# Kernel tuning notes

Hardware: AMD Instinct MI355X
Metric: run time of the kernel (lower is better)

The kernel has to match this reference:

```python
import jax, jax.numpy as jnp
import numpy as np

B, T, H, N_CLASSES = 2048, 128, 64, 32
N_STEPS = 10  # euler micro-steps over t in [0,1], step_size=0.1


def setup_inputs() -> dict:
    key = jax.random.key(0)
    ks = jax.random.split(key, 16)
    s = lambda fan_in: 1.0 / np.sqrt(fan_in)
    inp = {
        "times": jax.random.uniform(ks[0], (B, T), jnp.float32),
        "marks": jax.random.randint(ks[1], (B, T, 1), 0, N_CLASSES),
        "mask": jnp.ones((B, T), jnp.float32),
        # Diffeq.net: MLP(H+1 -> H -> H -> H), Tanh activations, Tanh final
        "W0": jax.random.uniform(ks[2], (H, H + 1), jnp.float32, -s(H + 1), s(H + 1)),
        "b0": jax.random.uniform(ks[3], (H,), jnp.float32, -s(H + 1), s(H + 1)),
        "W1": jax.random.uniform(ks[4], (H, H), jnp.float32, -s(H), s(H)),
        "b1": jax.random.uniform(ks[5], (H,), jnp.float32, -s(H), s(H)),
        "W2": jax.random.uniform(ks[6], (H, H), jnp.float32, -s(H), s(H)),
        "b2": jax.random.uniform(ks[7], (H,), jnp.float32, -s(H), s(H)),
        # Diffeq.intensity: Linear(H -> 1) + Softplus
        "Wi": jax.random.uniform(ks[8], (1, H), jnp.float32, -s(H), s(H)),
        "bi": jax.random.uniform(ks[9], (1,), jnp.float32, -s(H), s(H)) + 0.5,
        # Embedding(n_classes, H)
        "emb": jax.random.normal(ks[10], (N_CLASSES, H), jnp.float32),
        # LSTMCell(1+H, H)
        "W_ih": jax.random.uniform(ks[11], (4 * H, 1 + H), jnp.float32, -s(H), s(H)),
        "W_hh": jax.random.uniform(ks[12], (4 * H, H), jnp.float32, -s(H), s(H)),
        "b_ih": jax.random.uniform(ks[13], (4 * H,), jnp.float32, -s(H), s(H)),
        "b_hh": jax.random.uniform(ks[14], (4 * H,), jnp.float32, -s(H), s(H)),
    }
    return inp


def reference(times, marks, mask, W0, b0, W1, b1, W2, b2, Wi, bi, emb,
              W_ih, W_hh, b_ih, b_hh):
    dt = jnp.float32(1.0 / N_STEPS)

    def mlp(x):  # Diffeq.net
        x = jnp.tanh(x @ W0.T + b0)
        x = jnp.tanh(x @ W1.T + b1)
        return jnp.tanh(x @ W2.T + b2)

    def intensity(h):  # Diffeq.intensity (Softplus head) -> (B,1)
        return jax.nn.softplus(h @ Wi.T + bi)

    # faithful to original: marks[:, 1] is used at every timestep
    m1 = emb[marks[:, 1, 0]]  # (B,H)

    def step(carry, t_col):
        h, c = carry                       # (B,H), (B,H)
        t = t_col[:, None]                 # (B,1) -- diff (event time)
        # fixed-step euler solve of the Diffeq over s in [0,1]
        def euler(state, s):
            hh, integ = state
            s_t = (s * dt) * t             # (B,1) integration time scaled
            d_h = mlp(jnp.concatenate([s_t, hh], -1)) * t
            d_i = intensity(hh) * t
            return (hh + dt * d_h, integ + dt * d_i), None
        (h_ode, integ), _ = jax.lax.scan(
            euler, (h, jnp.zeros_like(t)),
            jnp.arange(N_STEPS, dtype=times.dtype))
        inten = intensity(h_ode)           # (B,1)
        # LSTMCell update with input [t, mark_embedding]
        x_in = jnp.concatenate([t, m1], -1)           # (B,1+H)
        gates = x_in @ W_ih.T + b_ih + h_ode @ W_hh.T + b_hh
        i_g, f_g, g_g, o_g = jnp.split(gates, 4, -1)
        c_new = jax.nn.sigmoid(f_g) * c + jax.nn.sigmoid(i_g) * jnp.tanh(g_g)
        h_new = jax.nn.sigmoid(o_g) * jnp.tanh(c_new)
        nll = (-jnp.log(inten) + integ)[:, 0]          # (B,)
        return (h_new, c_new), (h_ode, nll)

    h0 = jnp.zeros((times.shape[0], emb.shape[1]), times.dtype)
    _, (hidden, nll) = jax.lax.scan(step, (h0, h0), times.T)
    hidden = jnp.transpose(hidden, (1, 0, 2))   # (B,T,H)
    nll = nll.T                                  # (B,T)
    loss = (nll * mask).sum() / mask.sum()
    return loss, hidden
```

## Files before the change

### kernel.cpp

```cpp
#include <hip/hip_runtime.h>


#define T_LEN 128

typedef float  f32x4  __attribute__((ext_vector_type(4)));
typedef __bf16 bf16x8 __attribute__((ext_vector_type(8)));
typedef __bf16 bf16x2 __attribute__((ext_vector_type(2)));

#define MFMA16(a, b, c) __builtin_amdgcn_mfma_f32_16x16x32_bf16((a), (b), (c), 0, 0, 0)

__device__ __forceinline__ float rcp_f(float x) { return __builtin_amdgcn_rcpf(x); }
__device__ __forceinline__ float exp2_f(float x) { return __builtin_amdgcn_exp2f(x); }
__device__ __forceinline__ float log2_f(float x) { return __builtin_amdgcn_logf(x); }

constexpr float kL2E = 1.44269504088896340736f;
constexpr float kLN2 = 0.69314718055994530942f;

__device__ __forceinline__ float tanh_fast(float x) {
  float e = exp2_f(x * (2.0f * kL2E));
  return 1.0f - 2.0f * rcp_f(e + 1.0f);
}
__device__ __forceinline__ float sigm_fast(float x) {
  return rcp_f(1.0f + exp2_f(-kL2E * x));
}
__device__ __forceinline__ float softplus_fast(float x) {
  float neg = log2_f(1.0f + exp2_f(-kL2E * fabsf(x))) * kLN2;
  return fmaxf(x, 0.0f) + neg;
}
__device__ __forceinline__ unsigned packbf(float a, float b) {
  bf16x2 v; v[0] = (__bf16)a; v[1] = (__bf16)b;
  return __builtin_bit_cast(unsigned, v);
}

__launch_bounds__(256)
__global__ void jumpode_main(
    const float* __restrict__ times, const int* __restrict__ marks,
    const float* __restrict__ maskp, const float* __restrict__ W0,
    const float* __restrict__ b0,    const float* __restrict__ W1,
    const float* __restrict__ b1,    const float* __restrict__ W2,
    const float* __restrict__ b2,    const float* __restrict__ Wi,
    const float* __restrict__ bi,    const float* __restrict__ emb,
    const float* __restrict__ W_ih,  const float* __restrict__ W_hh,
    const float* __restrict__ b_ih,  const float* __restrict__ b_hh,
    float* __restrict__ out, float* __restrict__ ws)
{
  __shared__ __align__(16) unsigned whh_l[256 * 32];
  __shared__ __align__(16) float    gm1_l[8 * 256];
  __shared__ __align__(16) unsigned xbuf[2][16 * 32];
  __shared__ __align__(16) float    pint[16 * 4];
  __shared__ __align__(16) float    b0_l[64], b1_l[64], b2_l[64];
  __shared__ __align__(16) float    w0c0_l[64];
  __shared__ __align__(16) float    wihc0_l[256];
  __shared__ __align__(16) float    emb16[8][64];

  const int tid = threadIdx.x;
  const int wv  = tid >> 6;
  const int l   = tid & 63;
  const int b   = l & 15;
  const int q   = l >> 4;
  const int bm  = b & 7;
  const int row = blockIdx.x * 8 + bm;
  const int xsw = b & 7;

  if (tid < 64) {
    b0_l[tid] = b0[tid]; b1_l[tid] = b1[tid]; b2_l[tid] = b2[tid];
    w0c0_l[tid] = W0[tid * 65];
  }
  wihc0_l[tid] = W_ih[tid * 65];
  for (int idx = tid; idx < 512; idx += 256) {
    int rr = idx >> 6, cc = idx & 63;
    int mk = marks[(blockIdx.x * 8 + rr) * T_LEN + 1];
    emb16[rr][cc] = emb[mk * 64 + cc];
  }
  #pragma unroll 4
  for (int i = 0; i < 32; ++i) {
    int idx = i * 256 + tid;
    int rw = idx >> 5, c2 = idx & 31;
    unsigned pw = packbf(W_hh[rw * 64 + 2 * c2], W_hh[rw * 64 + 2 * c2 + 1]);
    int gr = c2 >> 2;
    whh_l[rw * 32 + ((gr ^ (rw & 7)) << 2) + (c2 & 3)] = pw;
  }
  __syncthreads();

  {
    int g = tid;
    float acc[8];
    #pragma unroll
    for (int bb = 0; bb < 8; ++bb) acc[bb] = 0.0f;
    const float* wr = &W_ih[g * 65 + 1];
    for (int k = 0; k < 64; ++k) {
      float w = wr[k];
      #pragma unroll
      for (int bb = 0; bb < 8; ++bb) acc[bb] += w * emb16[bb][k];
    }
    float bias = b_ih[g] + b_hh[g];
    int gg = g >> 2;
    #pragma unroll
    for (int bb = 0; bb < 8; ++bb)
      gm1_l[bb * 256 + ((gg ^ bb) << 2) + (g & 3)] = acc[bb] + bias;
  }

  bf16x8 w0f[2], w1f[2], w2f[2];
  {
    const int fm = 16 * wv + b;
    #pragma unroll
    for (int kt = 0; kt < 2; ++kt) {
      const float* r0 = &W0[fm * 65 + 1 + kt * 32 + q * 8];
      const float* r1 = &W1[fm * 64 +     kt * 32 + q * 8];
      const float* r2 = &W2[fm * 64 +     kt * 32 + q * 8];
      bf16x8 a, bb, c;
      #pragma unroll
      for (int e = 0; e < 8; ++e) {
        a[e] = (__bf16)r0[e]; bb[e] = (__bf16)r1[e]; c[e] = (__bf16)r2[e];
      }
      w0f[kt] = a; w1f[kt] = bb; w2f[kt] = c;
    }
  }
  f32x4 wiv;
  #pragma unroll
  for (int r = 0; r < 4; ++r) wiv[r] = Wi[16 * wv + 4 * q + r];
  const float bi_s = bi[0];
  const f32x4 b0v = *(const f32x4*)&b0_l[16 * wv + 4 * q];
  const f32x4 b1v = *(const f32x4*)&b1_l[16 * wv + 4 * q];
  const f32x4 b2v = *(const f32x4*)&b2_l[16 * wv + 4 * q];
  const f32x4 c0v = *(const f32x4*)&w0c0_l[16 * wv + 4 * q];
  __syncthreads();

  auto write_x = [&](unsigned* buf, const f32x4 v) {
    int gr = (2 * wv + (q >> 1)) ^ xsw;
    int wb = b * 32 + (gr << 2) + ((q & 1) << 1);
    buf[wb]     = packbf(v[0], v[1]);
    buf[wb + 1] = packbf(v[2], v[3]);
  };
  auto read_bfrag = [&](const unsigned* buf, int kt) -> bf16x8 {
    int gr = (kt * 4 + q) ^ xsw;
    return *(const bf16x8*)((const char*)buf + b * 128 + gr * 16);
  };
  auto whh_frag = [&](int R, int kt) -> bf16x8 {
    int rw = R * 16 + b;
    int gr = (kt * 4 + q) ^ xsw;
    return *(const bf16x8*)((const char*)whh_l + rw * 128 + gr * 16);
  };
  auto ld_gm1 = [&](int R) -> f32x4 {
    int gr = (R * 4 + q) ^ xsw;
    return *(const f32x4*)((const char*)gm1_l + bm * 1024 + gr * 16);
  };
  auto isect_partial = [&](const f32x4 v) {
    float part = wiv[0] * v[0] + wiv[1] * v[1] + wiv[2] * v[2] + wiv[3] * v[3];
    part += __shfl_xor(part, 16);
    part += __shfl_xor(part, 32);
    if (l < 16) pint[b * 4 + wv] = part;
  };

  f32x4 hst = (f32x4){0.f, 0.f, 0.f, 0.f};
  f32x4 cst = (f32x4){0.f, 0.f, 0.f, 0.f};
  float nll_acc = 0.f, m_acc = 0.f;
  const float sel0 = (q == 0 && b < 8) ? 1.0f : 0.0f;
  int xp = 0;

  #pragma unroll 1
  for (int step = 0; step < T_LEN; ++step) {
    const float tb  = times[row * T_LEN + step];
    const float dtt = 0.1f * tb;
    f32x4 hh = hst;
    float integ = 0.f;

    #pragma unroll 1
    for (int s = 0; s < 10; ++s) {
      isect_partial(hh);
      write_x(xbuf[xp], hh);
      __syncthreads();
      bf16x8 Bf0 = read_bfrag(xbuf[xp], 0), Bf1 = read_bfrag(xbuf[xp], 1);
      xp ^= 1;
      if (wv == 0) {
        f32x4 p = *(const f32x4*)&pint[b * 4];
        integ += dtt * softplus_fast(p[0] + p[1] + p[2] + p[3] + bi_s);
      }
      const float st = (float)s * dtt;

      f32x4 acc = (f32x4){0.f, 0.f, 0.f, 0.f};
      acc = MFMA16(w0f[0], Bf0, acc);
      acc = MFMA16(w0f[1], Bf1, acc);
      f32x4 y;
      #pragma unroll
      for (int r = 0; r < 4; ++r) y[r] = tanh_fast(acc[r] + b0v[r] + c0v[r] * st);
      write_x(xbuf[xp], y);
      __syncthreads();
      Bf0 = read_bfrag(xbuf[xp], 0); Bf1 = read_bfrag(xbuf[xp], 1);
      xp ^= 1;

      acc = (f32x4){0.f, 0.f, 0.f, 0.f};
      acc = MFMA16(w1f[0], Bf0, acc);
      acc = MFMA16(w1f[1], Bf1, acc);
      #pragma unroll
      for (int r = 0; r < 4; ++r) y[r] = tanh_fast(acc[r] + b1v[r]);
      write_x(xbuf[xp], y);
      __syncthreads();
      Bf0 = read_bfrag(xbuf[xp], 0); Bf1 = read_bfrag(xbuf[xp], 1);
      xp ^= 1;

      acc = (f32x4){0.f, 0.f, 0.f, 0.f};
      acc = MFMA16(w2f[0], Bf0, acc);
      acc = MFMA16(w2f[1], Bf1, acc);
      #pragma unroll
      for (int r = 0; r < 4; ++r) hh[r] += dtt * tanh_fast(acc[r] + b2v[r]);
    }

    isect_partial(hh);
    write_x(xbuf[xp], hh);
    if (b < 8) {
      size_t obase = 1 + (((size_t)row) * T_LEN + step) * 64 + 16 * wv + 4 * q;
      out[obase + 0] = hh[0]; out[obase + 1] = hh[1];
      out[obase + 2] = hh[2]; out[obase + 3] = hh[3];
    }
    __syncthreads();
    bf16x8 Bf0 = read_bfrag(xbuf[xp], 0), Bf1 = read_bfrag(xbuf[xp], 1);
    xp ^= 1;

    float nll = 0.f;
    if (wv == 0) {
      f32x4 p = *(const f32x4*)&pint[b * 4];
      float inten = softplus_fast(p[0] + p[1] + p[2] + p[3] + bi_s);
      nll = -(log2_f(inten) * kLN2) + integ;
    }

    f32x4 ga[4];
    #pragma unroll
    for (int g = 0; g < 4; ++g) {
      const int Rb = 4 * g + wv;
      f32x4 a = (f32x4){0.f, 0.f, 0.f, 0.f};
      a = MFMA16(whh_frag(Rb, 0), Bf0, a);
      a = MFMA16(whh_frag(Rb, 1), Bf1, a);
      f32x4 gm = ld_gm1(Rb);
      f32x4 wc = *(const f32x4*)&wihc0_l[Rb * 16 + q * 4];
      #pragma unroll
      for (int r = 0; r < 4; ++r) ga[g][r] = a[r] + gm[r] + wc[r] * tb;
    }
    #pragma unroll
    for (int r = 0; r < 4; ++r) {
      float ig = sigm_fast(ga[0][r]), fg = sigm_fast(ga[1][r]);
      float gg = tanh_fast(ga[2][r]), og = sigm_fast(ga[3][r]);
      float cn = fg * cst[r] + ig * gg;
      cst[r] = cn;
      hst[r] = og * tanh_fast(cn);
    }

    if (wv == 0) {
      float mval = maskp[row * T_LEN + step];
      nll_acc += sel0 * mval * nll;
      m_acc   += sel0 * mval;
    }
  }

  if (wv == 0) {
    #pragma unroll
    for (int off = 1; off < 64; off <<= 1) {
      nll_acc += __shfl_xor(nll_acc, off);
      m_acc   += __shfl_xor(m_acc, off);
    }
    if (tid == 0) {
      atomicAdd(&ws[0], nll_acc);
      atomicAdd(&ws[1], m_acc);
    }
  }
}

__global__ void jumpode_fin(const float* __restrict__ ws, float* __restrict__ out) {
  if (threadIdx.x == 0 && blockIdx.x == 0) out[0] = ws[0] / ws[1];
}

extern "C" void kernel_launch(void* const* d_in, const int* in_sizes, int n_in,
                              void* d_out, int out_size, void* d_ws, size_t ws_size,
                              hipStream_t stream) {
  (void)in_sizes; (void)n_in; (void)out_size; (void)ws_size;
  const float* times = (const float*)d_in[0];
  const int*   marks = (const int*)  d_in[1];
  const float* maskp = (const float*)d_in[2];
  const float* W0    = (const float*)d_in[3];
  const float* b0    = (const float*)d_in[4];
  const float* W1    = (const float*)d_in[5];
  const float* b1    = (const float*)d_in[6];
  const float* W2    = (const float*)d_in[7];
  const float* b2    = (const float*)d_in[8];
  const float* Wi    = (const float*)d_in[9];
  const float* bi    = (const float*)d_in[10];
  const float* emb   = (const float*)d_in[11];
  const float* W_ih  = (const float*)d_in[12];
  const float* W_hh  = (const float*)d_in[13];
  const float* b_ih  = (const float*)d_in[14];
  const float* b_hh  = (const float*)d_in[15];
  float* out = (float*)d_out;
  float* ws  = (float*)d_ws;

  (void)hipMemsetAsync(d_ws, 0, 2 * sizeof(float), stream);
  jumpode_main<<<dim3(256), dim3(256), 0, stream>>>(
      times, marks, maskp, W0, b0, W1, b1, W2, b2, Wi, bi, emb,
      W_ih, W_hh, b_ih, b_hh, out, ws);
  jumpode_fin<<<dim3(1), dim3(64), 0, stream>>>(ws, out);
}
```

Baseline: 1.006 ms.

## Halve batch rows per block to 4, double grid, fold biases into MFMA accumulators

Each block now handles 4 batch rows instead of 8, and the grid doubles to 512 blocks so more CUs take part in the serial recurrence. The 16-wide MFMA N dimension is now only a quarter used, but per-block latency is unchanged while the parallel spread over the 256 CUs doubles. Bias and time terms are preloaded into the MFMA accumulator input, which removes per-element adds after the matrix ops. The cost is that each block repeats its weight staging into LDS and registers, and less of each MFMA does useful work.

```diff
diff --git a/kernel.cpp b/kernel.cpp
--- a/kernel.cpp
+++ b/kernel.cpp
@@ -45,21 +45,21 @@
     float* __restrict__ out, float* __restrict__ ws)
 {
   __shared__ __align__(16) unsigned whh_l[256 * 32];
-  __shared__ __align__(16) float    gm1_l[8 * 256];
+  __shared__ __align__(16) float    gm1_l[4 * 256];
   __shared__ __align__(16) unsigned xbuf[2][16 * 32];
   __shared__ __align__(16) float    pint[16 * 4];
   __shared__ __align__(16) float    b0_l[64], b1_l[64], b2_l[64];
   __shared__ __align__(16) float    w0c0_l[64];
   __shared__ __align__(16) float    wihc0_l[256];
-  __shared__ __align__(16) float    emb16[8][64];
+  __shared__ __align__(16) float    emb16[4][64];
 
   const int tid = threadIdx.x;
   const int wv  = tid >> 6;
   const int l   = tid & 63;
   const int b   = l & 15;
   const int q   = l >> 4;
-  const int bm  = b & 7;
-  const int row = blockIdx.x * 8 + bm;
+  const int bm  = b & 3;
+  const int row = blockIdx.x * 4 + bm;
   const int xsw = b & 7;
 
   if (tid < 64) {
@@ -67,9 +67,9 @@
     w0c0_l[tid] = W0[tid * 65];
   }
   wihc0_l[tid] = W_ih[tid * 65];
-  for (int idx = tid; idx < 512; idx += 256) {
-    int rr = idx >> 6, cc = idx & 63;
-    int mk = marks[(blockIdx.x * 8 + rr) * T_LEN + 1];
+  if (tid < 256) {
+    int rr = tid >> 6, cc = tid & 63;
+    int mk = marks[(blockIdx.x * 4 + rr) * T_LEN + 1];
     emb16[rr][cc] = emb[mk * 64 + cc];
   }
   #pragma unroll 4
@@ -84,19 +84,19 @@
 
   {
     int g = tid;
-    float acc[8];
-    #pragma unroll
-    for (int bb = 0; bb < 8; ++bb) acc[bb] = 0.0f;
+    float acc[4];
+    #pragma unroll
+    for (int bb = 0; bb < 4; ++bb) acc[bb] = 0.0f;
     const float* wr = &W_ih[g * 65 + 1];
     for (int k = 0; k < 64; ++k) {
       float w = wr[k];
       #pragma unroll
-      for (int bb = 0; bb < 8; ++bb) acc[bb] += w * emb16[bb][k];
+      for (int bb = 0; bb < 4; ++bb) acc[bb] += w * emb16[bb][k];
     }
     float bias = b_ih[g] + b_hh[g];
     int gg = g >> 2;
     #pragma unroll
-    for (int bb = 0; bb < 8; ++bb)
+    for (int bb = 0; bb < 4; ++bb)
       gm1_l[bb * 256 + ((gg ^ bb) << 2) + (g & 3)] = acc[bb] + bias;
   }
 
@@ -142,7 +142,7 @@
     return *(const bf16x8*)((const char*)whh_l + rw * 128 + gr * 16);
   };
   auto ld_gm1 = [&](int R) -> f32x4 {
-    int gr = (R * 4 + q) ^ xsw;
+    int gr = (R * 4 + q) ^ bm;
     return *(const f32x4*)((const char*)gm1_l + bm * 1024 + gr * 16);
   };
   auto isect_partial = [&](const f32x4 v) {
@@ -155,7 +155,7 @@
   f32x4 hst = (f32x4){0.f, 0.f, 0.f, 0.f};
   f32x4 cst = (f32x4){0.f, 0.f, 0.f, 0.f};
   float nll_acc = 0.f, m_acc = 0.f;
-  const float sel0 = (q == 0 && b < 8) ? 1.0f : 0.0f;
+  const float sel0 = (q == 0 && b < 4) ? 1.0f : 0.0f;
   int xp = 0;
 
   #pragma unroll 1
@@ -178,37 +178,37 @@
       }
       const float st = (float)s * dtt;
 
-      f32x4 acc = (f32x4){0.f, 0.f, 0.f, 0.f};
-      acc = MFMA16(w0f[0], Bf0, acc);
+      f32x4 cin;
+      #pragma unroll
+      for (int r = 0; r < 4; ++r) cin[r] = b0v[r] + c0v[r] * st;
+      f32x4 acc = MFMA16(w0f[0], Bf0, cin);
       acc = MFMA16(w0f[1], Bf1, acc);
       f32x4 y;
       #pragma unroll
-      for (int r = 0; r < 4; ++r) y[r] = tanh_fast(acc[r] + b0v[r] + c0v[r] * st);
+      for (int r = 0; r < 4; ++r) y[r] = tanh_fast(acc[r]);
       write_x(xbuf[xp], y);
       __syncthreads();
       Bf0 = read_bfrag(xbuf[xp], 0); Bf1 = read_bfrag(xbuf[xp], 1);
       xp ^= 1;
 
-      acc = (f32x4){0.f, 0.f, 0.f, 0.f};
-      acc = MFMA16(w1f[0], Bf0, acc);
+      acc = MFMA16(w1f[0], Bf0, b1v);
       acc = MFMA16(w1f[1], Bf1, acc);
       #pragma unroll
-      for (int r = 0; r < 4; ++r) y[r] = tanh_fast(acc[r] + b1v[r]);
+      for (int r = 0; r < 4; ++r) y[r] = tanh_fast(acc[r]);
       write_x(xbuf[xp], y);
       __syncthreads();
       Bf0 = read_bfrag(xbuf[xp], 0); Bf1 = read_bfrag(xbuf[xp], 1);
       xp ^= 1;
 
-      acc = (f32x4){0.f, 0.f, 0.f, 0.f};
-      acc = MFMA16(w2f[0], Bf0, acc);
+      acc = MFMA16(w2f[0], Bf0, b2v);
       acc = MFMA16(w2f[1], Bf1, acc);
       #pragma unroll
-      for (int r = 0; r < 4; ++r) hh[r] += dtt * tanh_fast(acc[r] + b2v[r]);
+      for (int r = 0; r < 4; ++r) hh[r] += dtt * tanh_fast(acc[r]);
     }
 
     isect_partial(hh);
     write_x(xbuf[xp], hh);
-    if (b < 8) {
+    if (b < 4) {
       size_t obase = 1 + (((size_t)row) * T_LEN + step) * 64 + 16 * wv + 4 * q;
       out[obase + 0] = hh[0]; out[obase + 1] = hh[1];
       out[obase + 2] = hh[2]; out[obase + 3] = hh[3];
@@ -228,13 +228,13 @@
     #pragma unroll
     for (int g = 0; g < 4; ++g) {
       const int Rb = 4 * g + wv;
-      f32x4 a = (f32x4){0.f, 0.f, 0.f, 0.f};
-      a = MFMA16(whh_frag(Rb, 0), Bf0, a);
-      a = MFMA16(whh_frag(Rb, 1), Bf1, a);
       f32x4 gm = ld_gm1(Rb);
       f32x4 wc = *(const f32x4*)&wihc0_l[Rb * 16 + q * 4];
-      #pragma unroll
-      for (int r = 0; r < 4; ++r) ga[g][r] = a[r] + gm[r] + wc[r] * tb;
+      f32x4 cin;
+      #pragma unroll
+      for (int r = 0; r < 4; ++r) cin[r] = gm[r] + wc[r] * tb;
+      f32x4 a = MFMA16(whh_frag(Rb, 0), Bf0, cin);
+      ga[g] = MFMA16(whh_frag(Rb, 1), Bf1, a);
     }
     #pragma unroll
     for (int r = 0; r < 4; ++r) {
@@ -293,7 +293,7 @@
   float* ws  = (float*)d_ws;
 
   (void)hipMemsetAsync(d_ws, 0, 2 * sizeof(float), stream);
-  jumpode_main<<<dim3(256), dim3(256), 0, stream>>>(
+  jumpode_main<<<dim3(512), dim3(256), 0, stream>>>(
       times, marks, maskp, W0, b0, W1, b1, W2, b2, Wi, bi, emb,
       W_ih, W_hh, b_ih, b_hh, out, ws);
   jumpode_fin<<<dim3(1), dim3(64), 0, stream>>>(ws, out);
```

Result: slower. 1.222 ms (+21.4%).

## Restructure Euler substep with static buffers, bias-seeded MFMA, and preloaded times/mask

Applied to the files above, without the earlier changes.

The double-buffer index toggling is replaced by fixed ping-pong buffers, with each substep reusing its first buffer for the third layer. The Euler loop is unrolled by two so buffer addresses are compile-time constants. Biases and time terms are folded into the MFMA accumulator inputs, and the two K-halves use independent accumulators to shorten dependency chains. Times and mask are staged into LDS once at kernel start, which removes global loads from the serial loop. Softplus work is moved after the MFMA issue to overlap with it, at the cost of more LDS use and per-substep st accumulation instead of s*dtt.

```diff
diff --git a/kernel.cpp b/kernel.cpp
--- a/kernel.cpp
+++ b/kernel.cpp
@@ -46,12 +46,16 @@
 {
   __shared__ __align__(16) unsigned whh_l[256 * 32];
   __shared__ __align__(16) float    gm1_l[8 * 256];
-  __shared__ __align__(16) unsigned xbuf[2][16 * 32];
-  __shared__ __align__(16) float    pint[16 * 4];
+  __shared__ __align__(16) unsigned xb0[16 * 32];
+  __shared__ __align__(16) unsigned xb1[16 * 32];
+  __shared__ __align__(16) unsigned xb2[16 * 32];
+  __shared__ __align__(16) float    pint[3][16 * 4];
   __shared__ __align__(16) float    b0_l[64], b1_l[64], b2_l[64];
   __shared__ __align__(16) float    w0c0_l[64];
   __shared__ __align__(16) float    wihc0_l[256];
   __shared__ __align__(16) float    emb16[8][64];
+  __shared__ __align__(16) float    tim_l[8][T_LEN];
+  __shared__ __align__(16) float    msk_l[8][T_LEN];
 
   const int tid = threadIdx.x;
   const int wv  = tid >> 6;
@@ -71,6 +75,11 @@
     int rr = idx >> 6, cc = idx & 63;
     int mk = marks[(blockIdx.x * 8 + rr) * T_LEN + 1];
     emb16[rr][cc] = emb[mk * 64 + cc];
+  }
+  for (int idx = tid; idx < 1024; idx += 256) {
+    int rr = idx >> 7, cc = idx & 127;
+    tim_l[rr][cc] = times[(blockIdx.x * 8 + rr) * T_LEN + cc];
+    msk_l[rr][cc] = maskp[(blockIdx.x * 8 + rr) * T_LEN + cc];
   }
   #pragma unroll 4
   for (int i = 0; i < 32; ++i) {
@@ -124,6 +133,7 @@
   const f32x4 b1v = *(const f32x4*)&b1_l[16 * wv + 4 * q];
   const f32x4 b2v = *(const f32x4*)&b2_l[16 * wv + 4 * q];
   const f32x4 c0v = *(const f32x4*)&w0c0_l[16 * wv + 4 * q];
+  const f32x4 zf  = (f32x4){0.f, 0.f, 0.f, 0.f};
   __syncthreads();
 
   auto write_x = [&](unsigned* buf, const f32x4 v) {
@@ -142,99 +152,103 @@
     return *(const bf16x8*)((const char*)whh_l + rw * 128 + gr * 16);
   };
   auto ld_gm1 = [&](int R) -> f32x4 {
-    int gr = (R * 4 + q) ^ xsw;
+    int gr = (R * 4 + q) ^ bm;
     return *(const f32x4*)((const char*)gm1_l + bm * 1024 + gr * 16);
   };
-  auto isect_partial = [&](const f32x4 v) {
+  auto isect_partial = [&](float* pb, const f32x4 v) {
     float part = wiv[0] * v[0] + wiv[1] * v[1] + wiv[2] * v[2] + wiv[3] * v[3];
     part += __shfl_xor(part, 16);
     part += __shfl_xor(part, 32);
-    if (l < 16) pint[b * 4 + wv] = part;
-  };
-
-  f32x4 hst = (f32x4){0.f, 0.f, 0.f, 0.f};
-  f32x4 cst = (f32x4){0.f, 0.f, 0.f, 0.f};
+    if (l < 16) pb[b * 4 + wv] = part;
+  };
+
+  f32x4 hst = zf, cst = zf;
   float nll_acc = 0.f, m_acc = 0.f;
   const float sel0 = (q == 0 && b < 8) ? 1.0f : 0.0f;
-  int xp = 0;
+
+  f32x4 hh;
+  float integ, dtt, st, tb;
+
+  auto euler_substep = [&](unsigned* BA, unsigned* BB, float* PB) {
+    isect_partial(PB, hh);
+    write_x(BA, hh);
+    __syncthreads();
+    bf16x8 Bf0 = read_bfrag(BA, 0), Bf1 = read_bfrag(BA, 1);
+
+    f32x4 cin;
+    #pragma unroll
+    for (int r = 0; r < 4; ++r) cin[r] = b0v[r] + c0v[r] * st;
+    f32x4 a0 = MFMA16(w0f[0], Bf0, cin);
+    f32x4 a1 = MFMA16(w0f[1], Bf1, zf);
+    if (wv == 0) {
+      f32x4 p = *(const f32x4*)&PB[b * 4];
+      integ += dtt * softplus_fast(p[0] + p[1] + p[2] + p[3] + bi_s);
+    }
+    f32x4 y;
+    #pragma unroll
+    for (int r = 0; r < 4; ++r) y[r] = tanh_fast(a0[r] + a1[r]);
+    write_x(BB, y);
+    __syncthreads();
+    Bf0 = read_bfrag(BB, 0); Bf1 = read_bfrag(BB, 1);
+
+    a0 = MFMA16(w1f[0], Bf0, b1v);
+    a1 = MFMA16(w1f[1], Bf1, zf);
+    #pragma unroll
+    for (int r = 0; r < 4; ++r) y[r] = tanh_fast(a0[r] + a1[r]);
+    write_x(BA, y);
+    __syncthreads();
+    Bf0 = read_bfrag(BA, 0); Bf1 = read_bfrag(BA, 1);
+
+    a0 = MFMA16(w2f[0], Bf0, b2v);
+    a1 = MFMA16(w2f[1], Bf1, zf);
+    #pragma unroll
+    for (int r = 0; r < 4; ++r) hh[r] += dtt * tanh_fast(a0[r] + a1[r]);
+    st += dtt;
+  };
 
   #pragma unroll 1
   for (int step = 0; step < T_LEN; ++step) {
-    const float tb  = times[row * T_LEN + step];
-    const float dtt = 0.1f * tb;
-    f32x4 hh = hst;
-    float integ = 0.f;
+    tb  = tim_l[bm][step];
+    dtt = 0.1f * tb;
+    hh  = hst;
+    integ = 0.f;
+    st  = 0.f;
 
     #pragma unroll 1
-    for (int s = 0; s < 10; ++s) {
-      isect_partial(hh);
-      write_x(xbuf[xp], hh);
-      __syncthreads();
-      bf16x8 Bf0 = read_bfrag(xbuf[xp], 0), Bf1 = read_bfrag(xbuf[xp], 1);
-      xp ^= 1;
-      if (wv == 0) {
-        f32x4 p = *(const f32x4*)&pint[b * 4];
-        integ += dtt * softplus_fast(p[0] + p[1] + p[2] + p[3] + bi_s);
-      }
-      const float st = (float)s * dtt;
-
-      f32x4 acc = (f32x4){0.f, 0.f, 0.f, 0.f};
-      acc = MFMA16(w0f[0], Bf0, acc);
-      acc = MFMA16(w0f[1], Bf1, acc);
-      f32x4 y;
-      #pragma unroll
-      for (int r = 0; r < 4; ++r) y[r] = tanh_fast(acc[r] + b0v[r] + c0v[r] * st);
-      write_x(xbuf[xp], y);
-      __syncthreads();
-      Bf0 = read_bfrag(xbuf[xp], 0); Bf1 = read_bfrag(xbuf[xp], 1);
-      xp ^= 1;
-
-      acc = (f32x4){0.f, 0.f, 0.f, 0.f};
-      acc = MFMA16(w1f[0], Bf0, acc);
-      acc = MFMA16(w1f[1], Bf1, acc);
-      #pragma unroll
-      for (int r = 0; r < 4; ++r) y[r] = tanh_fast(acc[r] + b1v[r]);
-      write_x(xbuf[xp], y);
-      __syncthreads();
-      Bf0 = read_bfrag(xbuf[xp], 0); Bf1 = read_bfrag(xbuf[xp], 1);
-      xp ^= 1;
-
-      acc = (f32x4){0.f, 0.f, 0.f, 0.f};
-      acc = MFMA16(w2f[0], Bf0, acc);
-      acc = MFMA16(w2f[1], Bf1, acc);
-      #pragma unroll
-      for (int r = 0; r < 4; ++r) hh[r] += dtt * tanh_fast(acc[r] + b2v[r]);
-    }
-
-    isect_partial(hh);
-    write_x(xbuf[xp], hh);
+    for (int s2 = 0; s2 < 5; ++s2) {
+      euler_substep(xb0, xb1, pint[0]);
+      euler_substep(xb1, xb0, pint[1]);
+    }
+
+    isect_partial(pint[2], hh);
+    write_x(xb2, hh);
     if (b < 8) {
       size_t obase = 1 + (((size_t)row) * T_LEN + step) * 64 + 16 * wv + 4 * q;
       out[obase + 0] = hh[0]; out[obase + 1] = hh[1];
       out[obase + 2] = hh[2]; out[obase + 3] = hh[3];
     }
     __syncthreads();
-    bf16x8 Bf0 = read_bfrag(xbuf[xp], 0), Bf1 = read_bfrag(xbuf[xp], 1);
-    xp ^= 1;
-
-    float nll = 0.f;
-    if (wv == 0) {
-      f32x4 p = *(const f32x4*)&pint[b * 4];
-      float inten = softplus_fast(p[0] + p[1] + p[2] + p[3] + bi_s);
-      nll = -(log2_f(inten) * kLN2) + integ;
-    }
+    bf16x8 Bf0 = read_bfrag(xb2, 0), Bf1 = read_bfrag(xb2, 1);
 
     f32x4 ga[4];
     #pragma unroll
     for (int g = 0; g < 4; ++g) {
       const int Rb = 4 * g + wv;
-      f32x4 a = (f32x4){0.f, 0.f, 0.f, 0.f};
-      a = MFMA16(whh_frag(Rb, 0), Bf0, a);
-      a = MFMA16(whh_frag(Rb, 1), Bf1, a);
       f32x4 gm = ld_gm1(Rb);
       f32x4 wc = *(const f32x4*)&wihc0_l[Rb * 16 + q * 4];
+      f32x4 cin;
       #pragma unroll
-      for (int r = 0; r < 4; ++r) ga[g][r] = a[r] + gm[r] + wc[r] * tb;
+      for (int r = 0; r < 4; ++r) cin[r] = gm[r] + wc[r] * tb;
+      f32x4 a = MFMA16(whh_frag(Rb, 0), Bf0, cin);
+      ga[g] = MFMA16(whh_frag(Rb, 1), Bf1, a);
+    }
+    if (wv == 0) {
+      f32x4 p = *(const f32x4*)&pint[2][b * 4];
+      float inten = softplus_fast(p[0] + p[1] + p[2] + p[3] + bi_s);
+      float nll = -(log2_f(inten) * kLN2) + integ;
+      float mval = msk_l[bm][step];
+      nll_acc += sel0 * mval * nll;
+      m_acc   += sel0 * mval;
     }
     #pragma unroll
     for (int r = 0; r < 4; ++r) {
@@ -243,12 +257,6 @@
       float cn = fg * cst[r] + ig * gg;
       cst[r] = cn;
       hst[r] = og * tanh_fast(cn);
-    }
-
-    if (wv == 0) {
-      float mval = maskp[row * T_LEN + step];
-      nll_acc += sel0 * mval * nll;
-      m_acc   += sel0 * mval;
     }
   }
 
```

After: 1.006 ms. Within noise of the previous version (-0.0%).
